# Kernel optimization log

Hardware: AMD Instinct MI355X
Metric: run time of the kernel (lower is better)

The kernel has to match this reference:

```python
import jax, jax.numpy as jnp
import numpy as np

N, P, C, T, V = 32, 6, 128, 64, 25
S = 3        # num_subset
CI = 32      # inter_channels
EPS = 1e-5
NEG_SLOPE = 0.1


def conv1x1(x, w, b):
    # x: (N,P,Cin,T,V), w: (Cout,Cin), b: (Cout,)
    return jnp.einsum('npctv,oc->npotv', x, w) + b[None, None, :, None, None]


def batchnorm(x, gamma, beta):
    # training-mode BN over (N,P,T,V) per channel, matching torch forward math
    mu = x.mean(axis=(0, 1, 3, 4), keepdims=True)
    var = x.var(axis=(0, 1, 3, 4), keepdims=True)
    xh = (x - mu) * jax.lax.rsqrt(var + EPS)
    return xh * gamma[None, None, :, None, None] + beta[None, None, :, None, None]


def leaky(x):
    return jnp.where(x >= 0, x, NEG_SLOPE * x)


def t_block(inp, att_bias, alphat, w_in, b_in, w_out, b_out, g_out, be_out,
            w_ff, b_ff, g_ff, be_ff):
    n, p, c, t, v = inp.shape
    qk = conv1x1(inp, w_in, b_in)                       # (N,P,2*S*CI,T,V)
    qk = qk.reshape(n, p, 2, S, CI, t, v).transpose(2, 0, 3, 1, 4, 5, 6)
    q, k = qk[0], qk[1]                                 # (N,S,P,CI,T,V)
    scores = jnp.einsum('nspctv,nspcqv->nsptq', q, k) / (CI * v)
    att = att_bias + jnp.tanh(scores) * alphat          # (N,S,P,T,T)
    y = jnp.einsum('npctv,nsptq->nspcqv', inp, att)     # (N,S,P,C,T,V)
    y = y.transpose(0, 2, 1, 3, 4, 5).reshape(n, p, S * c, t, v)
    y = batchnorm(conv1x1(y, w_out, b_out), g_out, be_out)
    y = leaky(inp + y)                                  # residual (identity down path)
    y2 = batchnorm(conv1x1(y, w_ff, b_ff), g_ff, be_ff)
    return leaky(y + y2)


def setup_inputs() -> dict:
    key = jax.random.key(0)
    ks = jax.random.split(key, 8)
    sc = 0.05
    return {
        'x': jax.random.normal(ks[0], (N, P, C, T, V), jnp.float32),
        'att_t1': jnp.zeros((1, S, 1, T, T), jnp.float32),
        'att_t2': jnp.zeros((1, S, 1, T, T), jnp.float32),
        'alphat': jnp.ones((1, S, 1, 1, 1), jnp.float32),
        'w_in': jax.random.normal(ks[1], (2 * S * CI, C), jnp.float32) * sc,
        'b_in': jax.random.normal(ks[2], (2 * S * CI,), jnp.float32) * sc,
        'w_out': jax.random.normal(ks[3], (C, S * C), jnp.float32) * sc,
        'b_out': jax.random.normal(ks[4], (C,), jnp.float32) * sc,
        'g_out': jnp.ones((C,), jnp.float32),
        'be_out': jnp.zeros((C,), jnp.float32),
        'w_ff': jax.random.normal(ks[5], (C, C), jnp.float32) * sc,
        'b_ff': jax.random.normal(ks[6], (C,), jnp.float32) * sc,
        'g_ff': jnp.ones((C,), jnp.float32),
        'be_ff': jnp.zeros((C,), jnp.float32),
    }


def reference(x, att_t1, att_t2, alphat, w_in, b_in, w_out, b_out, g_out,
              be_out, w_ff, b_ff, g_ff, be_ff):
    y = t_block(x, att_t1, alphat, w_in, b_in, w_out, b_out, g_out, be_out,
                w_ff, b_ff, g_ff, be_ff)
    z = t_block(y, att_t2, alphat, w_in, b_in, w_out, b_out, g_out, be_out,
                w_ff, b_ff, g_ff, be_ff)
    return z
```

## Files before the change

kernel.cpp:

```cpp
#include <hip/hip_runtime.h>
#include <hip/hip_bf16.h>
#include <math.h>

#define NPB  192
#define CCH  128
#define TT   64
#define VV   25
#define PIX  1600
#define SS   3
#define EPC  307200.0f
static const size_t ETOT = (size_t)NPB * CCH * PIX;

typedef __attribute__((ext_vector_type(4))) float f32x4;
typedef __attribute__((ext_vector_type(8))) short short8;

__device__ __forceinline__ ushort f2bf(float f) {
    __hip_bfloat16 h = __float2bfloat16(f);
    return __builtin_bit_cast(unsigned short, h);
}
__device__ __forceinline__ float bf2f(ushort u) {
    unsigned int x = ((unsigned int)u) << 16;
    return __builtin_bit_cast(float, x);
}

__global__ void wprep(const float* __restrict__ w_in, const float* __restrict__ b_in,
                      const float* __restrict__ w_out, const float* __restrict__ w_ff,
                      ushort* __restrict__ Wp, float* __restrict__ bp,
                      ushort* __restrict__ Wo, ushort* __restrict__ Wf) {
    int i = blockIdx.x * 256 + threadIdx.x;
    if (i < 192 * 128) {
        int r = i >> 7, c = i & 127;
        int s = r / 64, j = r % 64;
        int src = (j < 32) ? (s * 32 + j) : (96 + s * 32 + (j - 32));
        Wp[i] = f2bf(w_in[src * 128 + c]);
        if (c == 0) bp[r] = b_in[src];
    }
    if (i < 128 * 384) Wo[i] = f2bf(w_out[i]);
    if (i < 128 * 128) Wf[i] = f2bf(w_ff[i]);
}

__global__ void remap_x(const float* __restrict__ x, ushort* __restrict__ xr) {
    size_t o = ((size_t)blockIdx.x * 256 + threadIdx.x) * 4;
    size_t row = o / PIX;
    int p = (int)(o % PIX);
    int v = p >> 6, t0 = p & 63;
    const float* xp = x + row * PIX;
    uint2 u;
    u.x = (uint)f2bf(xp[(t0 + 0) * 25 + v]) | ((uint)f2bf(xp[(t0 + 1) * 25 + v]) << 16);
    u.y = (uint)f2bf(xp[(t0 + 2) * 25 + v]) | ((uint)f2bf(xp[(t0 + 3) * 25 + v]) << 16);
    *(uint2*)(xr + o) = u;
}

__global__ __launch_bounds__(256)
void gemm_conv(const void* __restrict__ inp, int in_bf16,
               const ushort* __restrict__ W, int ldw,
               const float* __restrict__ bias,
               void* __restrict__ outp, int out_bf16, int out_ch,
               int accflag)
{
    __shared__ ushort Wt[64 * 72];
    __shared__ ushort Xt[128 * 72];
    const int np = blockIdx.x;
    const int pixbase = blockIdx.y * 128;
    const int obase = blockIdx.z * 64;
    const int tid = threadIdx.x;
    const int wave = tid >> 6, lane = tid & 63;
    const int quad = lane >> 4, l16 = lane & 15;
    const int wPix = wave * 32;

    f32x4 acc[4][2];
    if (accflag) {
        const float* op = (const float*)outp + ((size_t)np * out_ch + obase) * PIX + pixbase;
#pragma unroll
        for (int ms = 0; ms < 4; ++ms)
#pragma unroll
            for (int ns = 0; ns < 2; ++ns) {
                int pl = wPix + ns * 16 + l16;
                bool valid = (pixbase + pl) < PIX;
#pragma unroll
                for (int r = 0; r < 4; ++r) {
                    int ol = ms * 16 + quad * 4 + r;
                    acc[ms][ns][r] = valid ? op[(size_t)ol * PIX + pl] : 0.f;
                }
            }
    } else {
#pragma unroll
        for (int ms = 0; ms < 4; ++ms) {
            float bv[4];
#pragma unroll
            for (int r = 0; r < 4; ++r) {
                int ol = ms * 16 + quad * 4 + r;
                bv[r] = bias ? bias[obase + ol] : 0.f;
            }
#pragma unroll
            for (int ns = 0; ns < 2; ++ns)
#pragma unroll
                for (int r = 0; r < 4; ++r) acc[ms][ns][r] = bv[r];
        }
    }

    const ushort* inb = (const ushort*)inp;
    const float* inf = (const float*)inp;
    const size_t in_off = (size_t)np * 128 * PIX;

    for (int kc = 0; kc < 2; ++kc) {
        const int kbase = kc * 64;
        {
            int o = tid >> 2, seg = tid & 3;
            const ushort* src = W + (size_t)(obase + o) * ldw + kbase + seg * 16;
            uint4 a = *(const uint4*)src;
            uint4 b = *(const uint4*)(src + 8);
            *(uint4*)&Wt[o * 72 + seg * 16] = a;
            *(uint4*)&Wt[o * 72 + seg * 16 + 8] = b;
        }
        {
            int cp = tid & 31, rq = tid >> 5;
            int c = cp * 2;
            int p0 = rq * 16;
            bool valid = (pixbase + p0) < PIX;
            if (in_bf16) {
                uint ra[8], rb[8];
                if (valid) {
                    const ushort* s0 = inb + in_off + (size_t)(kbase + c) * PIX + pixbase + p0;
                    const ushort* s1 = s0 + PIX;
                    *(uint4*)&ra[0] = *(const uint4*)s0;
                    *(uint4*)&ra[4] = *(const uint4*)(s0 + 8);
                    *(uint4*)&rb[0] = *(const uint4*)s1;
                    *(uint4*)&rb[4] = *(const uint4*)(s1 + 8);
                } else {
#pragma unroll
                    for (int h = 0; h < 8; ++h) { ra[h] = 0; rb[h] = 0; }
                }
#pragma unroll
                for (int h = 0; h < 8; ++h) {
                    uint lo = ra[h], hi = rb[h];
                    *(uint*)&Xt[(p0 + 2 * h) * 72 + c] = (lo & 0xffffu) | (hi << 16);
                    *(uint*)&Xt[(p0 + 2 * h + 1) * 72 + c] = (lo >> 16) | (hi & 0xffff0000u);
                }
            } else {
                if (valid) {
                    const float* s0 = inf + in_off + (size_t)(kbase + c) * PIX + pixbase + p0;
                    const float* s1 = s0 + PIX;
#pragma unroll
                    for (int b4 = 0; b4 < 4; ++b4) {
                        float4 u = ((const float4*)s0)[b4];
                        float4 w4 = ((const float4*)s1)[b4];
                        int p = p0 + b4 * 4;
                        *(uint*)&Xt[(p + 0) * 72 + c] = (uint)f2bf(u.x) | ((uint)f2bf(w4.x) << 16);
                        *(uint*)&Xt[(p + 1) * 72 + c] = (uint)f2bf(u.y) | ((uint)f2bf(w4.y) << 16);
                        *(uint*)&Xt[(p + 2) * 72 + c] = (uint)f2bf(u.z) | ((uint)f2bf(w4.z) << 16);
                        *(uint*)&Xt[(p + 3) * 72 + c] = (uint)f2bf(u.w) | ((uint)f2bf(w4.w) << 16);
                    }
                } else {
#pragma unroll
                    for (int h = 0; h < 16; ++h) *(uint*)&Xt[(p0 + h) * 72 + c] = 0;
                }
            }
        }
        __syncthreads();
#pragma unroll
        for (int ks = 0; ks < 2; ++ks) {
            const int kk = ks * 32;
            short8 a[4], b[2];
#pragma unroll
            for (int ms = 0; ms < 4; ++ms)
                a[ms] = *(const short8*)&Wt[(ms * 16 + l16) * 72 + kk + quad * 8];
#pragma unroll
            for (int ns = 0; ns < 2; ++ns)
                b[ns] = *(const short8*)&Xt[(wPix + ns * 16 + l16) * 72 + kk + quad * 8];
#pragma unroll
            for (int ms = 0; ms < 4; ++ms)
#pragma unroll
                for (int ns = 0; ns < 2; ++ns)
                    acc[ms][ns] = __builtin_amdgcn_mfma_f32_16x16x32_bf16(a[ms], b[ns], acc[ms][ns], 0, 0, 0);
        }
        __syncthreads();
    }

    if (out_bf16) {
        ushort* op = (ushort*)outp + ((size_t)np * out_ch + obase) * PIX + pixbase;
#pragma unroll
        for (int ms = 0; ms < 4; ++ms)
#pragma unroll
            for (int ns = 0; ns < 2; ++ns) {
                int pl = wPix + ns * 16 + l16;
                if (pixbase + pl >= PIX) continue;
#pragma unroll
                for (int r = 0; r < 4; ++r) {
                    int ol = ms * 16 + quad * 4 + r;
                    op[(size_t)ol * PIX + pl] = f2bf(acc[ms][ns][r]);
                }
            }
    } else {
        float* op = (float*)outp + ((size_t)np * out_ch + obase) * PIX + pixbase;
#pragma unroll
        for (int ms = 0; ms < 4; ++ms)
#pragma unroll
            for (int ns = 0; ns < 2; ++ns) {
                int pl = wPix + ns * 16 + l16;
                if (pixbase + pl >= PIX) continue;
#pragma unroll
                for (int r = 0; r < 4; ++r) {
                    int ol = ms * 16 + quad * 4 + r;
                    op[(size_t)ol * PIX + pl] = acc[ms][ns][r];
                }
            }
    }
}

__global__ __launch_bounds__(256)
void scores_mfma(const ushort* __restrict__ qk, const float* __restrict__ attb,
                 const float* __restrict__ alphat, float* __restrict__ att)
{
    __shared__ ushort Qs[64 * 128];
    __shared__ ushort Ks[64 * 128];
    const int np = blockIdx.x, s = blockIdx.y, tid = threadIdx.x;
    const int wave = tid >> 6, lane = tid & 63;
    const int quad = lane >> 4, l16 = lane & 15;
    const int tH = (wave >> 1) * 32, qH = (wave & 1) * 32;
    const ushort* qb = qk + ((size_t)np * 192 + s * 64) * PIX;
    const ushort* kb = qb + (size_t)32 * PIX;

    const int side = wave >> 1;
    const int cil = (wave & 1) * 2 + (lane >> 5);
    const int t0 = (lane & 31) * 2;
    const ushort* sbase = (side ? kb : qb);
    ushort* dst = side ? Ks : Qs;

    f32x4 acc[2][2];
#pragma unroll
    for (int ms = 0; ms < 2; ++ms)
#pragma unroll
        for (int ns = 0; ns < 2; ++ns)
#pragma unroll
            for (int r = 0; r < 4; ++r) acc[ms][ns][r] = 0.f;

    for (int c = 0; c < 8; ++c) {
        __syncthreads();
        {
            const int ci = c * 4 + cil;
            const ushort* sb = sbase + (size_t)ci * PIX + t0;
            uint u[25];
#pragma unroll
            for (int v = 0; v < 25; ++v)
                u[v] = *(const uint*)(sb + v * 64);
            uint rA[16], rB[16];
#pragma unroll
            for (int w2 = 0; w2 < 12; ++w2) {
                uint a = u[2 * w2], b = u[2 * w2 + 1];
                rA[w2] = (a & 0xffffu) | (b << 16);
                rB[w2] = (a >> 16) | (b & 0xffff0000u);
            }
            rA[12] = u[24] & 0xffffu;  rB[12] = u[24] >> 16;
            rA[13] = 0u; rA[14] = 0u; rA[15] = 0u;
            rB[13] = 0u; rB[14] = 0u; rB[15] = 0u;
#pragma unroll
            for (int b4 = 0; b4 < 4; ++b4) {
                int blkA = (cil * 4 + b4) ^ (t0 & 7);
                int blkB = (cil * 4 + b4) ^ ((t0 + 1) & 7);
                uint4 wa, wb;
                wa.x = rA[b4 * 4 + 0]; wa.y = rA[b4 * 4 + 1];
                wa.z = rA[b4 * 4 + 2]; wa.w = rA[b4 * 4 + 3];
                wb.x = rB[b4 * 4 + 0]; wb.y = rB[b4 * 4 + 1];
                wb.z = rB[b4 * 4 + 2]; wb.w = rB[b4 * 4 + 3];
                *(uint4*)&dst[t0 * 128 + blkA * 8] = wa;
                *(uint4*)&dst[(t0 + 1) * 128 + blkB * 8] = wb;
            }
        }
        __syncthreads();
#pragma unroll
        for (int ks = 0; ks < 4; ++ks) {
            short8 a[2], b[2];
#pragma unroll
            for (int ms = 0; ms < 2; ++ms) {
                int t = tH + ms * 16 + l16;
                int blk = (ks * 4 + quad) ^ (t & 7);
                a[ms] = *(const short8*)&Qs[t * 128 + blk * 8];
            }
#pragma unroll
            for (int ns = 0; ns < 2; ++ns) {
                int q = qH + ns * 16 + l16;
                int blk = (ks * 4 + quad) ^ (q & 7);
                b[ns] = *(const short8*)&Ks[q * 128 + blk * 8];
            }
#pragma unroll
            for (int ms = 0; ms < 2; ++ms)
#pragma unroll
                for (int ns = 0; ns < 2; ++ns)
                    acc[ms][ns] = __builtin_amdgcn_mfma_f32_16x16x32_bf16(a[ms], b[ns], acc[ms][ns], 0, 0, 0);
        }
    }

    const float alpha = alphat[s];
    const int n = np / 6, p = np % 6;
    const float* bp2 = attb + (size_t)s * 4096;
    float* ap = att + ((size_t)(n * SS + s) * 6 + p) * 4096;
    const float inv = 1.0f / 800.0f;
#pragma unroll
    for (int ms = 0; ms < 2; ++ms)
#pragma unroll
        for (int ns = 0; ns < 2; ++ns) {
            int q = qH + ns * 16 + l16;
#pragma unroll
            for (int r = 0; r < 4; ++r) {
                int t = tH + ms * 16 + quad * 4 + r;
                ap[t * 64 + q] = bp2[t * 64 + q] + tanhf(acc[ms][ns][r] * inv) * alpha;
            }
        }
}

__global__ __launch_bounds__(256)
void attn_conv(const ushort* __restrict__ xr, const float* __restrict__ att,
               const ushort* __restrict__ Wo, const float* __restrict__ bias,
               float* __restrict__ Z)
{
    __shared__ ushort Xa[128 * 72];
    __shared__ ushort Ta[64 * 72];
    __shared__ ushort Wt[64 * 136];
    __shared__ ushort Ys[64 * 128];
    const int np = blockIdx.x, v = blockIdx.y, zo = blockIdx.z;
    const int tid = threadIdx.x;
    const int wave = tid >> 6, lane = tid & 63;
    const int quad = lane >> 4, l16 = lane & 15;
    const int mH = (wave & 1) * 64;
    const int oL = (wave & 1) * 32;
    const int qH = (wave >> 1) * 32;
    const int n = np / 6, p = np % 6;

    {
        int cc = tid >> 1, half = tid & 1;
        const ushort* src = xr + ((size_t)np * 128 + cc) * PIX + v * 64 + half * 32;
        uint4 a = *(const uint4*)src;
        uint4 b = *(const uint4*)(src + 8);
        uint4 c0 = *(const uint4*)(src + 16);
        uint4 d = *(const uint4*)(src + 24);
        *(uint4*)&Xa[cc * 72 + half * 32] = a;
        *(uint4*)&Xa[cc * 72 + half * 32 + 8] = b;
        *(uint4*)&Xa[cc * 72 + half * 32 + 16] = c0;
        *(uint4*)&Xa[cc * 72 + half * 32 + 24] = d;
    }

    f32x4 acc2[2][2];
#pragma unroll
    for (int ms2 = 0; ms2 < 2; ++ms2) {
        float bv[4];
#pragma unroll
        for (int r = 0; r < 4; ++r)
            bv[r] = bias[zo * 64 + oL + ms2 * 16 + quad * 4 + r];
#pragma unroll
        for (int ns = 0; ns < 2; ++ns)
#pragma unroll
            for (int r = 0; r < 4; ++r) acc2[ms2][ns][r] = bv[r];
    }

    for (int s = 0; s < SS; ++s) {
        __syncthreads();
        {
            int q = tid >> 2, seg = tid & 3;
            const float* ab = att + ((size_t)(n * SS + s) * 6 + p) * 4096;
#pragma unroll
            for (int i2 = 0; i2 < 8; ++i2) {
                int t0 = seg * 16 + i2 * 2;
                uint w = (uint)f2bf(ab[t0 * 64 + q]) | ((uint)f2bf(ab[(t0 + 1) * 64 + q]) << 16);
                *(uint*)&Ta[q * 72 + t0] = w;
            }
        }
        {
            int o = tid >> 2, seg = tid & 3;
            const ushort* wsrc = Wo + (size_t)(zo * 64 + o) * 384 + s * 128 + seg * 32;
            ushort* wd = &Wt[o * 136 + seg * 32];
            *(uint4*)wd = *(const uint4*)wsrc;
            *(uint4*)(wd + 8) = *(const uint4*)(wsrc + 8);
            *(uint4*)(wd + 16) = *(const uint4*)(wsrc + 16);
            *(uint4*)(wd + 24) = *(const uint4*)(wsrc + 24);
        }
        __syncthreads();
        f32x4 acc[4][2];
#pragma unroll
        for (int ms = 0; ms < 4; ++ms)
#pragma unroll
            for (int ns = 0; ns < 2; ++ns)
#pragma unroll
                for (int r = 0; r < 4; ++r) acc[ms][ns][r] = 0.f;
#pragma unroll
        for (int ks = 0; ks < 2; ++ks) {
            const int kk = ks * 32;
            short8 a[4], b[2];
#pragma unroll
            for (int ms = 0; ms < 4; ++ms)
                a[ms] = *(const short8*)&Xa[(mH + ms * 16 + l16) * 72 + kk + quad * 8];
#pragma unroll
            for (int ns = 0; ns < 2; ++ns)
                b[ns] = *(const short8*)&Ta[(qH + ns * 16 + l16) * 72 + kk + quad * 8];
#pragma unroll
            for (int ms = 0; ms < 4; ++ms)
#pragma unroll
                for (int ns = 0; ns < 2; ++ns)
                    acc[ms][ns] = __builtin_amdgcn_mfma_f32_16x16x32_bf16(a[ms], b[ns], acc[ms][ns], 0, 0, 0);
        }
#pragma unroll
        for (int ms = 0; ms < 4; ++ms)
#pragma unroll
            for (int ns = 0; ns < 2; ++ns) {
                int q = qH + ns * 16 + l16;
                int c0 = mH + ms * 16 + quad * 4;
                uint w0 = (uint)f2bf(acc[ms][ns][0]) | ((uint)f2bf(acc[ms][ns][1]) << 16);
                uint w1 = (uint)f2bf(acc[ms][ns][2]) | ((uint)f2bf(acc[ms][ns][3]) << 16);
                int blk = (c0 >> 3) ^ (q & 7);
                ushort* d = &Ys[q * 128 + blk * 8 + (c0 & 7)];
                *(uint*)d = w0;
                *(uint*)(d + 2) = w1;
            }
        __syncthreads();
#pragma unroll
        for (int ks2 = 0; ks2 < 4; ++ks2) {
            short8 a2[2], b2[2];
#pragma unroll
            for (int ms2 = 0; ms2 < 2; ++ms2)
                a2[ms2] = *(const short8*)&Wt[(oL + ms2 * 16 + l16) * 136 + ks2 * 32 + quad * 8];
#pragma unroll
            for (int ns = 0; ns < 2; ++ns) {
                int q = qH + ns * 16 + l16;
                int blk = (ks2 * 4 + quad) ^ (q & 7);
                b2[ns] = *(const short8*)&Ys[q * 128 + blk * 8];
            }
#pragma unroll
            for (int ms2 = 0; ms2 < 2; ++ms2)
#pragma unroll
                for (int ns = 0; ns < 2; ++ns)
                    acc2[ms2][ns] = __builtin_amdgcn_mfma_f32_16x16x32_bf16(a2[ms2], b2[ns], acc2[ms2][ns], 0, 0, 0);
        }
    }

    float* zp = Z + ((size_t)np * 128 + zo * 64) * PIX + v * 64;
#pragma unroll
    for (int ms2 = 0; ms2 < 2; ++ms2)
#pragma unroll
        for (int ns = 0; ns < 2; ++ns) {
            int q = qH + ns * 16 + l16;
#pragma unroll
            for (int r = 0; r < 4; ++r) {
                int o = oL + ms2 * 16 + quad * 4 + r;
                zp[(size_t)o * PIX + q] = acc2[ms2][ns][r];
            }
        }
}

__global__ void bn_stats(const float* __restrict__ z, float* __restrict__ stats) {
    const int c = blockIdx.x, np = blockIdx.y, tid = threadIdx.x;
    const float* zp = z + ((size_t)np * CCH + c) * PIX;
    float s = 0.f, s2 = 0.f;
    for (int i = tid; i < PIX; i += 256) {
        float v = zp[i];
        s += v; s2 += v * v;
    }
    for (int off = 32; off; off >>= 1) {
        s += __shfl_down(s, off);
        s2 += __shfl_down(s2, off);
    }
    __shared__ float ls[4], ls2[4];
    const int w = tid >> 6, lane = tid & 63;
    if (lane == 0) { ls[w] = s; ls2[w] = s2; }
    __syncthreads();
    if (tid == 0) {
        s = ls[0] + ls[1] + ls[2] + ls[3];
        s2 = ls2[0] + ls2[1] + ls2[2] + ls2[3];
        atomicAdd(&stats[c], s);
        atomicAdd(&stats[128 + c], s2);
    }
}

__global__ void bn_finalize(const float* __restrict__ stats, const float* __restrict__ g,
                            const float* __restrict__ be, float* __restrict__ scsh) {
    const int c = threadIdx.x;
    float mean = stats[c] * (1.0f / EPC);
    float var = stats[128 + c] * (1.0f / EPC) - mean * mean;
    float inv = rsqrtf(var + 1e-5f);
    float sc = g[c] * inv;
    scsh[c] = sc;
    scsh[128 + c] = be[c] - mean * sc;
}

__global__ void res_bn_g(const float* __restrict__ x, const float* __restrict__ z,
                         const float* __restrict__ scsh, float* __restrict__ out) {
    size_t i = ((size_t)blockIdx.x * 256 + threadIdx.x) * 4;
    size_t row = i / PIX;
    int p = (int)(i % PIX);
    int ch = (int)(row & 127);
    float sc = scsh[ch], sh = scsh[128 + ch];
    const float* zr = z + row * PIX;
    float4 a = *(const float4*)(x + i);
    float xin[4] = {a.x, a.y, a.z, a.w};
    float4 r;
    float ro[4];
#pragma unroll
    for (int j = 0; j < 4; ++j) {
        int pp = p + j;
        int t = pp / 25, vv = pp - t * 25;
        float zz = zr[vv * 64 + t];
        float val = xin[j] + fmaf(zz, sc, sh);
        ro[j] = val >= 0.f ? val : 0.1f * val;
    }
    r.x = ro[0]; r.y = ro[1]; r.z = ro[2]; r.w = ro[3];
    *(float4*)(out + i) = r;
}

__global__ void res_bn_l(const float4* __restrict__ xr, const float4* __restrict__ zr,
                         const float* __restrict__ scsh, float4* __restrict__ out) {
    int i = blockIdx.x * 256 + threadIdx.x;
    int row = i / 400;
    int ch = row & 127;
    float sc = scsh[ch], sh = scsh[128 + ch];
    float4 a = xr[i], b = zr[i], r;
    r.x = a.x + fmaf(b.x, sc, sh);
    r.y = a.y + fmaf(b.y, sc, sh);
    r.z = a.z + fmaf(b.z, sc, sh);
    r.w = a.w + fmaf(b.w, sc, sh);
    r.x = r.x >= 0.f ? r.x : 0.1f * r.x;
    r.y = r.y >= 0.f ? r.y : 0.1f * r.y;
    r.z = r.z >= 0.f ? r.z : 0.1f * r.z;
    r.w = r.w >= 0.f ? r.w : 0.1f * r.w;
    out[i] = r;
}

struct Ctx {
    ushort *xr, *Wp, *Wo, *Wf;
    float *bp;
    float *R1, *R0, *ATT, *STATS;
    const float *alphat, *b_out, *g_out, *be_out, *b_ff, *g_ff, *be_ff;
};

static void run_block(const float* X, const float* attb, float* OUT,
                      const Ctx& c, hipStream_t stream) {
    const int EG = 38400;
    remap_x<<<EG, 256, 0, stream>>>(X, c.xr);
    gemm_conv<<<dim3(NPB, 13, 3), 256, 0, stream>>>(c.xr, 1, c.Wp, 128, c.bp,
                                                    (void*)c.R1, 1, 192, 0);
    scores_mfma<<<dim3(NPB, 3), 256, 0, stream>>>((const ushort*)c.R1, attb, c.alphat, c.ATT);
    attn_conv<<<dim3(NPB, VV, 2), 256, 0, stream>>>(c.xr, c.ATT, c.Wo, c.b_out, c.R0);
    hipMemsetAsync(c.STATS, 0, 256 * sizeof(float), stream);
    bn_stats<<<dim3(CCH, NPB), 256, 0, stream>>>(c.R0, c.STATS);
    bn_finalize<<<1, 128, 0, stream>>>(c.STATS, c.g_out, c.be_out, c.STATS + 256);
    res_bn_g<<<EG, 256, 0, stream>>>(X, c.R0, c.STATS + 256, c.R1);
    gemm_conv<<<dim3(NPB, 13, 2), 256, 0, stream>>>(c.R1, 0, c.Wf, 128, c.b_ff,
                                                    (void*)c.R0, 0, 128, 0);
    hipMemsetAsync(c.STATS, 0, 256 * sizeof(float), stream);
    bn_stats<<<dim3(CCH, NPB), 256, 0, stream>>>(c.R0, c.STATS);
    bn_finalize<<<1, 128, 0, stream>>>(c.STATS, c.g_ff, c.be_ff, c.STATS + 256);
    res_bn_l<<<EG, 256, 0, stream>>>((const float4*)c.R1, (const float4*)c.R0,
                                     c.STATS + 256, (float4*)OUT);
}

extern "C" void kernel_launch(void* const* d_in, const int* in_sizes, int n_in,
                              void* d_out, int out_size, void* d_ws, size_t ws_size,
                              hipStream_t stream) {
    const float* x = (const float*)d_in[0];
    const float* att1 = (const float*)d_in[1];
    const float* att2 = (const float*)d_in[2];
    Ctx c;
    c.alphat = (const float*)d_in[3];
    const float* w_in = (const float*)d_in[4];
    const float* b_in = (const float*)d_in[5];
    const float* w_out = (const float*)d_in[6];
    c.b_out = (const float*)d_in[7];
    c.g_out = (const float*)d_in[8];
    c.be_out = (const float*)d_in[9];
    const float* w_ff = (const float*)d_in[10];
    c.b_ff = (const float*)d_in[11];
    c.g_ff = (const float*)d_in[12];
    c.be_ff = (const float*)d_in[13];

    char* ws = (char*)d_ws;
    size_t off = 0;
    c.xr = (ushort*)(ws + off);   off += ETOT * 2;
    c.R1 = (float*)(ws + off);    off += ETOT * 4;
    c.R0 = (float*)(ws + off);    off += ETOT * 4;
    c.ATT = (float*)(ws + off);   off += (size_t)32 * 3 * 6 * 4096 * 4;
    c.STATS = (float*)(ws + off); off += 512 * 4;
    c.Wp = (ushort*)(ws + off);   off += 192 * 128 * 2;
    c.bp = (float*)(ws + off);    off += 192 * 4;
    c.Wo = (ushort*)(ws + off);   off += 128 * 384 * 2;
    c.Wf = (ushort*)(ws + off);   off += 128 * 128 * 2;

    wprep<<<192, 256, 0, stream>>>(w_in, b_in, w_out, w_ff, c.Wp, c.bp, c.Wo, c.Wf);

    float* out = (float*)d_out;
    run_block(x, att1, out, c, stream);
    run_block(out, att2, out, c, stream);
}
```

Measured before the change: 1.663 ms.

## Swizzle attn_conv LDS, load Wo fragments from global, feed FF conv bf16 copy

attn_conv drops padded shared-memory rows in favour of XOR-swizzled 64-wide rows for X and the attention tile. The attention tile is now loaded with a transposed per-lane pattern. The output-projection weights are read straight from global memory into register fragments instead of being staged through LDS, and launch bounds request 4 blocks per CU. res_bn_g also writes a bf16 copy of its output so the following FF conv can read bf16 input instead of fp32. This trades extra register pressure and an extra bf16 store for less LDS traffic and smaller reads in the FF GEMM.

```diff
diff --git a/kernel.cpp b/kernel.cpp
--- a/kernel.cpp
+++ b/kernel.cpp
@@ -309,14 +309,13 @@
         }
 }
 
-__global__ __launch_bounds__(256)
+__global__ __launch_bounds__(256, 4)
 void attn_conv(const ushort* __restrict__ xr, const float* __restrict__ att,
                const ushort* __restrict__ Wo, const float* __restrict__ bias,
                float* __restrict__ Z)
 {
-    __shared__ ushort Xa[128 * 72];
-    __shared__ ushort Ta[64 * 72];
-    __shared__ ushort Wt[64 * 136];
+    __shared__ ushort Xa[128 * 64];
+    __shared__ ushort Ta[64 * 64];
     __shared__ ushort Ys[64 * 128];
     const int np = blockIdx.x, v = blockIdx.y, zo = blockIdx.z;
     const int tid = threadIdx.x;
@@ -334,10 +333,12 @@
         uint4 b = *(const uint4*)(src + 8);
         uint4 c0 = *(const uint4*)(src + 16);
         uint4 d = *(const uint4*)(src + 24);
-        *(uint4*)&Xa[cc * 72 + half * 32] = a;
-        *(uint4*)&Xa[cc * 72 + half * 32 + 8] = b;
-        *(uint4*)&Xa[cc * 72 + half * 32 + 16] = c0;
-        *(uint4*)&Xa[cc * 72 + half * 32 + 24] = d;
+        int sw = cc & 7;
+        ushort* xb = &Xa[cc * 64];
+        *(uint4*)&xb[((half * 4 + 0) ^ sw) * 8] = a;
+        *(uint4*)&xb[((half * 4 + 1) ^ sw) * 8] = b;
+        *(uint4*)&xb[((half * 4 + 2) ^ sw) * 8] = c0;
+        *(uint4*)&xb[((half * 4 + 3) ^ sw) * 8] = d;
     }
 
     f32x4 acc2[2][2];
@@ -356,23 +357,25 @@
     for (int s = 0; s < SS; ++s) {
         __syncthreads();
         {
-            int q = tid >> 2, seg = tid & 3;
-            const float* ab = att + ((size_t)(n * SS + s) * 6 + p) * 4096;
-#pragma unroll
-            for (int i2 = 0; i2 < 8; ++i2) {
-                int t0 = seg * 16 + i2 * 2;
-                uint w = (uint)f2bf(ab[t0 * 64 + q]) | ((uint)f2bf(ab[(t0 + 1) * 64 + q]) << 16);
-                *(uint*)&Ta[q * 72 + t0] = w;
-            }
-        }
-        {
-            int o = tid >> 2, seg = tid & 3;
-            const ushort* wsrc = Wo + (size_t)(zo * 64 + o) * 384 + s * 128 + seg * 32;
-            ushort* wd = &Wt[o * 136 + seg * 32];
-            *(uint4*)wd = *(const uint4*)wsrc;
-            *(uint4*)(wd + 8) = *(const uint4*)(wsrc + 8);
-            *(uint4*)(wd + 16) = *(const uint4*)(wsrc + 16);
-            *(uint4*)(wd + 24) = *(const uint4*)(wsrc + 24);
+            const float* ab = att + ((size_t)(n * SS + s) * 6 + p) * 4096
+                              + (size_t)(wave * 16) * 64 + lane;
+            ushort tv[16];
+#pragma unroll
+            for (int i = 0; i < 16; ++i)
+                tv[i] = f2bf(ab[i * 64]);
+            uint4 wlo, whi;
+            wlo.x = (uint)tv[0] | ((uint)tv[1] << 16);
+            wlo.y = (uint)tv[2] | ((uint)tv[3] << 16);
+            wlo.z = (uint)tv[4] | ((uint)tv[5] << 16);
+            wlo.w = (uint)tv[6] | ((uint)tv[7] << 16);
+            whi.x = (uint)tv[8] | ((uint)tv[9] << 16);
+            whi.y = (uint)tv[10] | ((uint)tv[11] << 16);
+            whi.z = (uint)tv[12] | ((uint)tv[13] << 16);
+            whi.w = (uint)tv[14] | ((uint)tv[15] << 16);
+            int sw = lane & 7;
+            ushort* tb = &Ta[lane * 64];
+            *(uint4*)&tb[((wave * 2 + 0) ^ sw) * 8] = wlo;
+            *(uint4*)&tb[((wave * 2 + 1) ^ sw) * 8] = whi;
         }
         __syncthreads();
         f32x4 acc[4][2];
@@ -384,14 +387,19 @@
                 for (int r = 0; r < 4; ++r) acc[ms][ns][r] = 0.f;
 #pragma unroll
         for (int ks = 0; ks < 2; ++ks) {
-            const int kk = ks * 32;
             short8 a[4], b[2];
 #pragma unroll
-            for (int ms = 0; ms < 4; ++ms)
-                a[ms] = *(const short8*)&Xa[(mH + ms * 16 + l16) * 72 + kk + quad * 8];
-#pragma unroll
-            for (int ns = 0; ns < 2; ++ns)
-                b[ns] = *(const short8*)&Ta[(qH + ns * 16 + l16) * 72 + kk + quad * 8];
+            for (int ms = 0; ms < 4; ++ms) {
+                int row = mH + ms * 16 + l16;
+                int blk = (ks * 4 + quad) ^ (l16 & 7);
+                a[ms] = *(const short8*)&Xa[row * 64 + blk * 8];
+            }
+#pragma unroll
+            for (int ns = 0; ns < 2; ++ns) {
+                int row = qH + ns * 16 + l16;
+                int blk = (ks * 4 + quad) ^ (l16 & 7);
+                b[ns] = *(const short8*)&Ta[row * 64 + blk * 8];
+            }
 #pragma unroll
             for (int ms = 0; ms < 4; ++ms)
 #pragma unroll
@@ -412,12 +420,18 @@
                 *(uint*)(d + 2) = w1;
             }
         __syncthreads();
+        short8 wf[2][4];
+        {
+            const ushort* wb = Wo + (size_t)(zo * 64 + oL + l16) * 384 + s * 128 + quad * 8;
+#pragma unroll
+            for (int ms2 = 0; ms2 < 2; ++ms2)
+#pragma unroll
+                for (int ks2 = 0; ks2 < 4; ++ks2)
+                    wf[ms2][ks2] = *(const short8*)(wb + ms2 * 16 * 384 + ks2 * 32);
+        }
 #pragma unroll
         for (int ks2 = 0; ks2 < 4; ++ks2) {
-            short8 a2[2], b2[2];
-#pragma unroll
-            for (int ms2 = 0; ms2 < 2; ++ms2)
-                a2[ms2] = *(const short8*)&Wt[(oL + ms2 * 16 + l16) * 136 + ks2 * 32 + quad * 8];
+            short8 b2[2];
 #pragma unroll
             for (int ns = 0; ns < 2; ++ns) {
                 int q = qH + ns * 16 + l16;
@@ -428,7 +442,7 @@
             for (int ms2 = 0; ms2 < 2; ++ms2)
 #pragma unroll
                 for (int ns = 0; ns < 2; ++ns)
-                    acc2[ms2][ns] = __builtin_amdgcn_mfma_f32_16x16x32_bf16(a2[ms2], b2[ns], acc2[ms2][ns], 0, 0, 0);
+                    acc2[ms2][ns] = __builtin_amdgcn_mfma_f32_16x16x32_bf16(wf[ms2][ks2], b2[ns], acc2[ms2][ns], 0, 0, 0);
         }
     }
 
@@ -482,7 +496,8 @@
 }
 
 __global__ void res_bn_g(const float* __restrict__ x, const float* __restrict__ z,
-                         const float* __restrict__ scsh, float* __restrict__ out) {
+                         const float* __restrict__ scsh, float* __restrict__ out,
+                         ushort* __restrict__ outb) {
     size_t i = ((size_t)blockIdx.x * 256 + threadIdx.x) * 4;
     size_t row = i / PIX;
     int p = (int)(i % PIX);
@@ -503,6 +518,10 @@
     }
     r.x = ro[0]; r.y = ro[1]; r.z = ro[2]; r.w = ro[3];
     *(float4*)(out + i) = r;
+    uint2 ub;
+    ub.x = (uint)f2bf(ro[0]) | ((uint)f2bf(ro[1]) << 16);
+    ub.y = (uint)f2bf(ro[2]) | ((uint)f2bf(ro[3]) << 16);
+    *(uint2*)(outb + i) = ub;
 }
 
 __global__ void res_bn_l(const float4* __restrict__ xr, const float4* __restrict__ zr,
@@ -541,8 +560,8 @@
     hipMemsetAsync(c.STATS, 0, 256 * sizeof(float), stream);
     bn_stats<<<dim3(CCH, NPB), 256, 0, stream>>>(c.R0, c.STATS);
     bn_finalize<<<1, 128, 0, stream>>>(c.STATS, c.g_out, c.be_out, c.STATS + 256);
-    res_bn_g<<<EG, 256, 0, stream>>>(X, c.R0, c.STATS + 256, c.R1);
-    gemm_conv<<<dim3(NPB, 13, 2), 256, 0, stream>>>(c.R1, 0, c.Wf, 128, c.b_ff,
+    res_bn_g<<<EG, 256, 0, stream>>>(X, c.R0, c.STATS + 256, c.R1, c.xr);
+    gemm_conv<<<dim3(NPB, 13, 2), 256, 0, stream>>>(c.xr, 1, c.Wf, 128, c.b_ff,
                                                     (void*)c.R0, 0, 128, 0);
     hipMemsetAsync(c.STATS, 0, 256 * sizeof(float), stream);
     bn_stats<<<dim3(CCH, NPB), 256, 0, stream>>>(c.R0, c.STATS);
```

Result: faster. 1.583 ms (-4.8%).
